# Performance work log

Measured on AMD Instinct MI355X. Metric: run time of the kernel, lower is better.

Reference implementation:

```python
import jax, jax.numpy as jnp
import numpy as np

FEW_SHOT_K = 5
NUM_CLASSES = 3
SUPPORT_SIZE = 100


def setup_inputs() -> dict:
    key = jax.random.key(0)
    ks = jax.random.split(key, 12)
    B, S, H = 64, 512, 1024
    scale = 0.02
    return {
        "hidden_states": jax.random.normal(ks[0], (B, S, H), jnp.float32),
        "labels": jax.random.randint(ks[1], (B,), 0, NUM_CLASSES),
        "support_features": jax.random.normal(ks[2], (SUPPORT_SIZE, H), jnp.float32),
        "support_labels": jax.random.randint(ks[3], (SUPPORT_SIZE,), 0, NUM_CLASSES),
        "W_sim": jax.random.normal(ks[4], (128, H), jnp.float32) * scale,
        "b_sim": jnp.zeros((128,), jnp.float32),
        "W_div": jax.random.normal(ks[5], (128, H), jnp.float32) * scale,
        "b_div": jnp.zeros((128,), jnp.float32),
        "W_meta": jax.random.normal(ks[6], (H, H), jnp.float32) * scale,
        "b_meta": jnp.zeros((H,), jnp.float32),
        "W_con": jax.random.normal(ks[7], (256, H), jnp.float32) * scale,
        "b_con": jnp.zeros((256,), jnp.float32),
    }


def reference(hidden_states, labels, support_features, support_labels,
              W_sim, b_sim, W_div, b_div, W_meta, b_meta, W_con, b_con):
    B, S, H = hidden_states.shape
    pooled = hidden_states.mean(axis=1)                       # [B,H] sentence/query features
    similarity_features = pooled @ W_sim.T + b_sim            # [B,128]
    diversity_features = pooled @ W_div.T + b_div             # [B,128]
    meta = jnp.einsum('bsh,oh->bso', hidden_states, W_meta) + b_meta  # [B,S,H]
    meta_contrastive = meta.mean(axis=1) @ W_con.T + b_con    # [B,256]

    # update_support_set: circular buffer write starting at ptr=0, B<100 -> plain slice.
    # Features are .detach()'d in torch before storage.
    supF = support_features.at[:B].set(jax.lax.stop_gradient(pooled))
    supL = support_labels.at[:B].set(labels)

    # topk similarity + softmax weights
    sims = pooled @ supF.T                                    # [B,100]
    top_v, top_i = jax.lax.top_k(sims, FEW_SHOT_K)            # [B,K]
    weights = jax.nn.softmax(top_v, axis=1)                   # [B,K]
    sel_labels = supL[top_i]                                  # [B,K]

    # vectorized replacement of the per-element python scatter loop:
    # pred[b,c] = sum_i weights[b,i] * [sel_labels[b,i] == c], 0<=label<3 guard
    # jax.nn.one_hot yields all-zeros for out-of-range labels, matching the guard.
    onehot = jax.nn.one_hot(sel_labels, NUM_CLASSES, dtype=weights.dtype)  # [B,K,3]
    pred = jnp.einsum('bkc,bk->bc', onehot, weights)          # [B,3]
    few_shot_predictions = jnp.broadcast_to(pred[:, None, :], (B, S, NUM_CLASSES))

    return few_shot_predictions, similarity_features, diversity_features, meta_contrastive
```

## Files before the change

kernel.cpp:

```cpp
#include <hip/hip_runtime.h>

#define BB 64
#define SS 512
#define HH 1024
#define SUP 100
#define KFS 5
#define NCLS 3
#define SEG 32
#define KSPLIT 8
#define KB (HH / KSPLIT)
#define KC 32
#define ASLD 68

typedef float vfloat4 __attribute__((ext_vector_type(4)));

#define MAC16() { \
    _Pragma("unroll") \
    for (int k = 0; k < KC; ++k) { \
        float4 a4 = *(const float4*)&As[k][tm*4]; \
        float4 b4 = *(const float4*)&Bs[k][tn*4]; \
        acc[0][0]+=a4.x*b4.x; acc[0][1]+=a4.x*b4.y; acc[0][2]+=a4.x*b4.z; acc[0][3]+=a4.x*b4.w; \
        acc[1][0]+=a4.y*b4.x; acc[1][1]+=a4.y*b4.y; acc[1][2]+=a4.y*b4.z; acc[1][3]+=a4.y*b4.w; \
        acc[2][0]+=a4.z*b4.x; acc[2][1]+=a4.z*b4.y; acc[2][2]+=a4.z*b4.z; acc[2][3]+=a4.z*b4.w; \
        acc[3][0]+=a4.w*b4.x; acc[3][1]+=a4.w*b4.y; acc[3][2]+=a4.w*b4.z; acc[3][3]+=a4.w*b4.w; } }

#define WRITE_AS(s0, s1) { \
    As[lq*4+0][lr]=s0.x; As[lq*4+1][lr]=s0.y; As[lq*4+2][lr]=s0.z; As[lq*4+3][lr]=s0.w; \
    As[16+lq*4+0][lr]=s1.x; As[16+lq*4+1][lr]=s1.y; As[16+lq*4+2][lr]=s1.z; As[16+lq*4+3][lr]=s1.w; }

#define WRITE_BS(w0, w1) { \
    Bs[lq*4+0][lr]=w0.x; Bs[lq*4+1][lr]=w0.y; Bs[lq*4+2][lr]=w0.z; Bs[lq*4+3][lr]=w0.w; \
    Bs[16+lq*4+0][lr]=w1.x; Bs[16+lq*4+1][lr]=w1.y; Bs[16+lq*4+2][lr]=w1.z; Bs[16+lq*4+3][lr]=w1.w; }

#define STORE_OUT(buf, N) { \
    _Pragma("unroll") \
    for (int i = 0; i < 4; ++i) \
        *(float4*)((buf) + ((size_t)ks*64 + tm*4 + i)*(N) + n0 + tn*4) = \
            make_float4(acc[i][0], acc[i][1], acc[i][2], acc[i][3]); }

__global__ void pool_partial(const float* __restrict__ hs, float* __restrict__ part) {
    int blk = blockIdx.x;
    int b   = blk >> 5;
    int seg = blk & (SEG - 1);
    int t   = threadIdx.x;
    const vfloat4* src = (const vfloat4*)(hs + (size_t)b * SS * HH) + (size_t)(seg * 16) * 256 + t;
    vfloat4 v[16];
#pragma unroll
    for (int i = 0; i < 16; ++i) v[i] = __builtin_nontemporal_load(&src[(size_t)i * 256]);
#pragma unroll
    for (int st = 8; st; st >>= 1)
#pragma unroll
        for (int i = 0; i < st; ++i) v[i] += v[i + st];
    ((vfloat4*)part)[(size_t)(seg * BB + b) * 256 + t] = v[0];
}

__global__ void pool_reduce(const float* __restrict__ part, float* __restrict__ pooled) {
    int b = blockIdx.x;
    int t = threadIdx.x;
    float4 acc = make_float4(0.f, 0.f, 0.f, 0.f);
#pragma unroll 4
    for (int seg = 0; seg < SEG; ++seg) {
        float4 v = ((const float4*)part)[(size_t)(seg * BB + b) * 256 + t];
        acc.x += v.x; acc.y += v.y; acc.z += v.z; acc.w += v.w;
    }
    const float inv = 1.0f / 512.0f;
    acc.x *= inv; acc.y *= inv; acc.z *= inv; acc.w *= inv;
    ((float4*)pooled)[b * 256 + t] = acc;
}

__device__ __forceinline__ void gemm64_partial(const float* __restrict__ A,
                                               const float* __restrict__ W,
                                               float* __restrict__ partOut, int N,
                                               int n0, int k0, int ks, int t,
                                               float (*As)[ASLD], float (*Bs)[ASLD]) {
    int tm = t >> 4, tn = t & 15;
    int lr = t >> 2, lq = t & 3;
    float acc[4][4] = {};
    for (int kc = 0; kc < KB; kc += KC) {
        int ka = k0 + kc + lq * 4;
        float4 a0 = *(const float4*)(A + (size_t)lr * HH + ka);
        float4 a1 = *(const float4*)(A + (size_t)lr * HH + ka + 16);
        float4 w0 = *(const float4*)(W + (size_t)(n0 + lr) * HH + ka);
        float4 w1 = *(const float4*)(W + (size_t)(n0 + lr) * HH + ka + 16);
        WRITE_AS(a0, a1);
        WRITE_BS(w0, w1);
        __syncthreads();
        MAC16();
        __syncthreads();
    }
    STORE_OUT(partOut, N);
}

__global__ void lin_partial(const float* __restrict__ pooled,
                            const float* __restrict__ W_sim,
                            const float* __restrict__ W_div,
                            const float* __restrict__ W_met,
                            const float* __restrict__ supF,
                            float* __restrict__ pSim, float* __restrict__ pDiv,
                            float* __restrict__ pMet, float* __restrict__ pSims) {
    __shared__ __align__(16) float As[KC][ASLD];
    __shared__ __align__(16) float Bs[KC][ASLD];
    int id = blockIdx.x, t = threadIdx.x;

    if (id < 16) {
        gemm64_partial(pooled, W_sim, pSim, 128, (id >> 3) * 64, (id & 7) * KB, id & 7, t, As, Bs);
        return;
    }
    if (id < 32) {
        int i2 = id - 16;
        gemm64_partial(pooled, W_div, pDiv, 128, (i2 >> 3) * 64, (i2 & 7) * KB, i2 & 7, t, As, Bs);
        return;
    }
    if (id < 160) {
        int i2 = id - 32;
        gemm64_partial(pooled, W_met, pMet, 1024, (i2 >> 3) * 64, (i2 & 7) * KB, i2 & 7, t, As, Bs);
        return;
    }

    {
        int i2 = id - 160;
        int n0 = (i2 >> 3) * 64, ks = i2 & 7, k0 = ks * KB;
        int tm = t >> 4, tn = t & 15;
        int lr = t >> 2, lq = t & 3;
        float acc[4][4] = {};
        int j = n0 + lr;
        const float* wrow = (j < BB) ? (pooled + (size_t)j * HH)
                                     : (supF + (size_t)(j < SUP ? j : SUP - 1) * HH);
        for (int kc = 0; kc < KB; kc += KC) {
            int ka = k0 + kc + lq * 4;
            float4 a0 = *(const float4*)(pooled + (size_t)lr * HH + ka);
            float4 a1 = *(const float4*)(pooled + (size_t)lr * HH + ka + 16);
            float4 w0 = *(const float4*)(wrow + ka);
            float4 w1 = *(const float4*)(wrow + ka + 16);
            WRITE_AS(a0, a1);
            WRITE_BS(w0, w1);
            __syncthreads();
            MAC16();
            __syncthreads();
        }
        STORE_OUT(pSims, 128);
    }
}

__global__ void k4_tail(const float* __restrict__ pSims,
                        const int* __restrict__ labels,
                        const int* __restrict__ supL,
                        const float* __restrict__ pMet,
                        const float* __restrict__ b_met,
                        const float* __restrict__ W_con,
                        float* __restrict__ pCon,
                        float* __restrict__ out_fsp) {
    __shared__ __align__(16) float As[KC][ASLD];
    __shared__ __align__(16) float Bs[KC][ASLD];
    __shared__ float simsS[128];
    __shared__ float pred[NCLS];
    int blk = blockIdx.x, t = threadIdx.x;

    if (blk >= BB) {
        int id = blk - BB;
        int n0 = (id >> 3) * 64, ks = id & 7, k0 = ks * KB;
        int tm = t >> 4, tn = t & 15;
        int lr = t >> 2, lq = t & 3;
        float acc[4][4] = {};
        for (int kc = 0; kc < KB; kc += KC) {
            int ka = k0 + kc + lq * 4;
            float4 s0 = *(const float4*)(b_met + ka);
            float4 s1 = *(const float4*)(b_met + ka + 16);
#pragma unroll
            for (int p = 0; p < KSPLIT; ++p) {
                float4 v0 = *(const float4*)(pMet + ((size_t)p * 64 + lr) * HH + ka);
                float4 v1 = *(const float4*)(pMet + ((size_t)p * 64 + lr) * HH + ka + 16);
                s0.x += v0.x; s0.y += v0.y; s0.z += v0.z; s0.w += v0.w;
                s1.x += v1.x; s1.y += v1.y; s1.z += v1.z; s1.w += v1.w;
            }
            float4 w0 = *(const float4*)(W_con + (size_t)(n0 + lr) * HH + ka);
            float4 w1 = *(const float4*)(W_con + (size_t)(n0 + lr) * HH + ka + 16);
            WRITE_AS(s0, s1);
            WRITE_BS(w0, w1);
            __syncthreads();
            MAC16();
            __syncthreads();
        }
        STORE_OUT(pCon, 256);
        return;
    }

    int b = blk;
    if (t < 128) {
        float s = 0.f;
#pragma unroll
        for (int ks = 0; ks < KSPLIT; ++ks)
            s += pSims[((size_t)ks * 64 + b) * 128 + t];
        simsS[t] = s;
    }
    __syncthreads();

    if (t == 0) {
        float vals[KFS]; int idx[KFS];
        for (int i = 0; i < KFS; ++i) {
            float best = -3.4e38f; int bi = 0;
            for (int j = 0; j < SUP; ++j) {
                bool taken = false;
                for (int p = 0; p < i; ++p) taken = taken || (idx[p] == j);
                if (!taken && simsS[j] > best) { best = simsS[j]; bi = j; }
            }
            vals[i] = best; idx[i] = bi;
        }
        float mx = vals[0];
        for (int i = 1; i < KFS; ++i) mx = fmaxf(mx, vals[i]);
        float e[KFS], sum = 0.f;
        for (int i = 0; i < KFS; ++i) { e[i] = __expf(vals[i] - mx); sum += e[i]; }
        float p0 = 0.f, p1 = 0.f, p2 = 0.f;
        for (int i = 0; i < KFS; ++i) {
            int j = idx[i];
            int lab = (j < BB) ? labels[j] : supL[j];
            float wv = e[i] / sum;
            if (lab == 0) p0 += wv;
            else if (lab == 1) p1 += wv;
            else if (lab == 2) p2 += wv;
        }
        pred[0] = p0; pred[1] = p1; pred[2] = p2;
    }
    __syncthreads();

    float p[NCLS] = {pred[0], pred[1], pred[2]};
    for (int i = t; i < SS * NCLS; i += 256) {
        int c = i - (i / NCLS) * NCLS;
        out_fsp[(size_t)b * SS * NCLS + i] = p[c];
    }
}

__global__ void combine(const float* __restrict__ pSim, const float* __restrict__ b_sim,
                        const float* __restrict__ pDiv, const float* __restrict__ b_div,
                        const float* __restrict__ pCon, const float* __restrict__ b_con,
                        float* __restrict__ out_sim, float* __restrict__ out_div,
                        float* __restrict__ out_con) {
    int gid = blockIdx.x * 256 + threadIdx.x;
    if (gid < 8192) {
        float s = b_sim[gid & 127];
#pragma unroll
        for (int p = 0; p < KSPLIT; ++p) s += pSim[p * 8192 + gid];
        out_sim[gid] = s;
    } else if (gid < 16384) {
        int i = gid - 8192;
        float s = b_div[i & 127];
#pragma unroll
        for (int p = 0; p < KSPLIT; ++p) s += pDiv[p * 8192 + i];
        out_div[i] = s;
    } else {
        int i = gid - 16384;
        float s = b_con[i & 255];
#pragma unroll
        for (int p = 0; p < KSPLIT; ++p) s += pCon[p * 16384 + i];
        out_con[i] = s;
    }
}

extern "C" void kernel_launch(void* const* d_in, const int* in_sizes, int n_in,
                              void* d_out, int out_size, void* d_ws, size_t ws_size,
                              hipStream_t stream) {
    const float* hs    = (const float*)d_in[0];
    const int*   lab   = (const int*)  d_in[1];
    const float* supF  = (const float*)d_in[2];
    const int*   supL  = (const int*)  d_in[3];
    const float* W_sim = (const float*)d_in[4];
    const float* b_sim = (const float*)d_in[5];
    const float* W_div = (const float*)d_in[6];
    const float* b_div = (const float*)d_in[7];
    const float* W_met = (const float*)d_in[8];
    const float* b_met = (const float*)d_in[9];
    const float* W_con = (const float*)d_in[10];
    const float* b_con = (const float*)d_in[11];

    float* out = (float*)d_out;
    float* out_fsp = out;
    float* out_sim = out + 98304;
    float* out_div = out + 106496;
    float* out_con = out + 114688;

    float* ws     = (float*)d_ws;
    float* part   = ws;
    float* pooled = part + (size_t)SEG * BB * HH;
    float* pSim   = pooled + BB * HH;
    float* pDiv   = pSim + (size_t)KSPLIT * BB * 128;
    float* pMet   = pDiv + (size_t)KSPLIT * BB * 128;
    float* pCon   = pMet + (size_t)KSPLIT * BB * HH;
    float* pSims  = pCon + (size_t)KSPLIT * BB * 256;

    pool_partial<<<BB * SEG, 256, 0, stream>>>(hs, part);
    pool_reduce <<<BB,       256, 0, stream>>>(part, pooled);
    lin_partial <<<176,      256, 0, stream>>>(pooled, W_sim, W_div, W_met, supF,
                                               pSim, pDiv, pMet, pSims);
    k4_tail     <<<96,       256, 0, stream>>>(pSims, lab, supL, pMet, b_met, W_con,
                                               pCon, out_fsp);
    combine     <<<128,      256, 0, stream>>>(pSim, b_sim, pDiv, b_div, pCon, b_con,
                                               out_sim, out_div, out_con);
}
```

Baseline: 73.09 us.

## Fold combine kernel into k4_tail and drop split-K for contrastive GEMM

Removes the separate combine launch by having the 64 per-batch tail blocks also reduce the sim/div split-K partials with bias. The W_con GEMM now runs as 4 blocks over the full K=1024, writing out_con directly with bias instead of 32 split-K blocks plus a later reduction. It also replaces nontemporal vector loads in pool_partial with plain float4 loads. This saves one launch and a partial-buffer round trip, but the contrastive GEMM has much less parallelism and each of its blocks runs a far longer K loop.

```diff
diff --git a/kernel.cpp b/kernel.cpp
--- a/kernel.cpp
+++ b/kernel.cpp
@@ -12,8 +12,6 @@
 #define KC 32
 #define ASLD 68
 
-typedef float vfloat4 __attribute__((ext_vector_type(4)));
-
 #define MAC16() { \
     _Pragma("unroll") \
     for (int k = 0; k < KC; ++k) { \
@@ -43,15 +41,18 @@
     int b   = blk >> 5;
     int seg = blk & (SEG - 1);
     int t   = threadIdx.x;
-    const vfloat4* src = (const vfloat4*)(hs + (size_t)b * SS * HH) + (size_t)(seg * 16) * 256 + t;
-    vfloat4 v[16];
-#pragma unroll
-    for (int i = 0; i < 16; ++i) v[i] = __builtin_nontemporal_load(&src[(size_t)i * 256]);
+    const float4* src = (const float4*)(hs + (size_t)b * SS * HH) + (size_t)(seg * 16) * 256 + t;
+    float4 v[16];
+#pragma unroll
+    for (int i = 0; i < 16; ++i) v[i] = src[(size_t)i * 256];
 #pragma unroll
     for (int st = 8; st; st >>= 1)
 #pragma unroll
-        for (int i = 0; i < st; ++i) v[i] += v[i + st];
-    ((vfloat4*)part)[(size_t)(seg * BB + b) * 256 + t] = v[0];
+        for (int i = 0; i < st; ++i) {
+            v[i].x += v[i + st].x; v[i].y += v[i + st].y;
+            v[i].z += v[i + st].z; v[i].w += v[i + st].w;
+        }
+    ((float4*)part)[(size_t)(seg * BB + b) * 256 + t] = v[0];
 }
 
 __global__ void pool_reduce(const float* __restrict__ part, float* __restrict__ pooled) {
@@ -148,8 +149,11 @@
                         const float* __restrict__ pMet,
                         const float* __restrict__ b_met,
                         const float* __restrict__ W_con,
-                        float* __restrict__ pCon,
-                        float* __restrict__ out_fsp) {
+                        const float* __restrict__ b_con,
+                        const float* __restrict__ pSim, const float* __restrict__ b_sim,
+                        const float* __restrict__ pDiv, const float* __restrict__ b_div,
+                        float* __restrict__ out_fsp, float* __restrict__ out_sim,
+                        float* __restrict__ out_div, float* __restrict__ out_con) {
     __shared__ __align__(16) float As[KC][ASLD];
     __shared__ __align__(16) float Bs[KC][ASLD];
     __shared__ float simsS[128];
@@ -158,12 +162,12 @@
 
     if (blk >= BB) {
         int id = blk - BB;
-        int n0 = (id >> 3) * 64, ks = id & 7, k0 = ks * KB;
+        int n0 = id * 64;
         int tm = t >> 4, tn = t & 15;
         int lr = t >> 2, lq = t & 3;
         float acc[4][4] = {};
-        for (int kc = 0; kc < KB; kc += KC) {
-            int ka = k0 + kc + lq * 4;
+        for (int kc = 0; kc < HH; kc += KC) {
+            int ka = kc + lq * 4;
             float4 s0 = *(const float4*)(b_met + ka);
             float4 s1 = *(const float4*)(b_met + ka + 16);
 #pragma unroll
@@ -181,7 +185,12 @@
             MAC16();
             __syncthreads();
         }
-        STORE_OUT(pCon, 256);
+        float4 bc = *(const float4*)(b_con + n0 + tn * 4);
+#pragma unroll
+        for (int i = 0; i < 4; ++i)
+            *(float4*)(out_con + (size_t)(tm * 4 + i) * 256 + n0 + tn * 4) =
+                make_float4(acc[i][0] + bc.x, acc[i][1] + bc.y,
+                            acc[i][2] + bc.z, acc[i][3] + bc.w);
         return;
     }
 
@@ -228,31 +237,21 @@
         int c = i - (i / NCLS) * NCLS;
         out_fsp[(size_t)b * SS * NCLS + i] = p[c];
     }
-}
-
-__global__ void combine(const float* __restrict__ pSim, const float* __restrict__ b_sim,
-                        const float* __restrict__ pDiv, const float* __restrict__ b_div,
-                        const float* __restrict__ pCon, const float* __restrict__ b_con,
-                        float* __restrict__ out_sim, float* __restrict__ out_div,
-                        float* __restrict__ out_con) {
-    int gid = blockIdx.x * 256 + threadIdx.x;
-    if (gid < 8192) {
-        float s = b_sim[gid & 127];
-#pragma unroll
-        for (int p = 0; p < KSPLIT; ++p) s += pSim[p * 8192 + gid];
-        out_sim[gid] = s;
-    } else if (gid < 16384) {
-        int i = gid - 8192;
-        float s = b_div[i & 127];
-#pragma unroll
-        for (int p = 0; p < KSPLIT; ++p) s += pDiv[p * 8192 + i];
-        out_div[i] = s;
-    } else {
-        int i = gid - 16384;
-        float s = b_con[i & 255];
-#pragma unroll
-        for (int p = 0; p < KSPLIT; ++p) s += pCon[p * 16384 + i];
-        out_con[i] = s;
+
+    {
+        int i = b * 256 + t;
+        if (i < 8192) {
+            float s = b_sim[i & 127];
+#pragma unroll
+            for (int p2 = 0; p2 < KSPLIT; ++p2) s += pSim[p2 * 8192 + i];
+            out_sim[i] = s;
+        } else {
+            int i2 = i - 8192;
+            float s = b_div[i2 & 127];
+#pragma unroll
+            for (int p2 = 0; p2 < KSPLIT; ++p2) s += pDiv[p2 * 8192 + i2];
+            out_div[i2] = s;
+        }
     }
 }
 
@@ -284,15 +283,13 @@
     float* pSim   = pooled + BB * HH;
     float* pDiv   = pSim + (size_t)KSPLIT * BB * 128;
     float* pMet   = pDiv + (size_t)KSPLIT * BB * 128;
-    float* pCon   = pMet + (size_t)KSPLIT * BB * HH;
-    float* pSims  = pCon + (size_t)KSPLIT * BB * 256;
+    float* pSims  = pMet + (size_t)KSPLIT * BB * HH;
 
     pool_partial<<<BB * SEG, 256, 0, stream>>>(hs, part);
     pool_reduce <<<BB,       256, 0, stream>>>(part, pooled);
     lin_partial <<<176,      256, 0, stream>>>(pooled, W_sim, W_div, W_met, supF,
                                                pSim, pDiv, pMet, pSims);
-    k4_tail     <<<96,       256, 0, stream>>>(pSims, lab, supL, pMet, b_met, W_con,
-                                               pCon, out_fsp);
-    combine     <<<128,      256, 0, stream>>>(pSim, b_sim, pDiv, b_div, pCon, b_con,
-                                               out_sim, out_div, out_con);
-}
+    k4_tail     <<<BB + 4,   256, 0, stream>>>(pSims, lab, supL, pMet, b_met,
+                                               W_con, b_con, pSim, b_sim, pDiv, b_div,
+                                               out_fsp, out_sim, out_div, out_con);
+}
```

Result: slower. 135.6 us (+85.5%).
